# Kernel tuning notes

Measured on AMD Instinct MI355X. Metric: run time of the kernel, lower is better.

The kernel has to match this reference:

```python
import jax, jax.numpy as jnp
import numpy as np
import math

B, T, DIM = 2, 2048, 4096
N_HEADS, N_KV_HEADS = 32, 8
HEAD_DIM = DIM // N_HEADS          # 128
N_REP = N_HEADS // N_KV_HEADS      # 4
ROPE_THETA = 500000.0
NEG_INF = -1e9


def setup_inputs() -> dict:
    key = jax.random.key(0)
    ks = jax.random.split(key, 5)
    x = jax.random.normal(ks[0], (B, T, DIM), dtype=jnp.float32)
    # rotary angles: theta_j = pos * base^(-2j/d), shape [T, HEAD_DIM//2]
    inv_freq = 1.0 / (ROPE_THETA ** (jnp.arange(0, HEAD_DIM, 2, dtype=jnp.float32) / HEAD_DIM))
    freqs = jnp.arange(T, dtype=jnp.float32)[:, None] * inv_freq[None, :]
    # causal additive mask [T, T]
    mask = jnp.where(jnp.tril(jnp.ones((T, T), dtype=bool)), 0.0, NEG_INF).astype(jnp.float32)
    s = 0.02
    wq = jax.random.normal(ks[1], (DIM, N_HEADS * HEAD_DIM), dtype=jnp.float32) * s
    wk = jax.random.normal(ks[2], (DIM, N_KV_HEADS * HEAD_DIM), dtype=jnp.float32) * s
    wv = jax.random.normal(ks[3], (DIM, N_KV_HEADS * HEAD_DIM), dtype=jnp.float32) * s
    wo = jax.random.normal(ks[4], (N_HEADS * HEAD_DIM, DIM), dtype=jnp.float32) * s
    return {"x": x, "freqs": freqs, "mask": mask, "wq": wq, "wk": wk, "wv": wv, "wo": wo, "start_pos": 0}


def _apply_rope(x, cos, sin):
    # x: [B, T, H, D]; cos/sin: [T, D//2]; adjacent pairs rotated (view-as-complex)
    xr = x[..., 0::2]
    xi = x[..., 1::2]
    c = cos[None, :, None, :]
    s = sin[None, :, None, :]
    out_r = xr * c - xi * s
    out_i = xr * s + xi * c
    return jnp.stack([out_r, out_i], axis=-1).reshape(x.shape)


def reference(x, freqs, mask, wq, wk, wv, wo, start_pos):
    Bx, Tx, C = x.shape
    xq = (x @ wq).reshape(Bx, Tx, N_HEADS, HEAD_DIM)
    xk = (x @ wk).reshape(Bx, Tx, N_KV_HEADS, HEAD_DIM)
    xv = (x @ wv).reshape(Bx, Tx, N_KV_HEADS, HEAD_DIM)
    cos, sin = jnp.cos(freqs), jnp.sin(freqs)
    xq = _apply_rope(xq, cos, sin)
    xk = _apply_rope(xk, cos, sin)
    # repeat_kv for GQA: [B, T, Hkv, D] -> [B, T, Hkv*n_rep, D]
    xk = jnp.repeat(xk, N_REP, axis=2)
    xv = jnp.repeat(xv, N_REP, axis=2)
    q = xq.transpose(0, 2, 1, 3)  # [B, H, T, D]
    k = xk.transpose(0, 2, 1, 3)
    v = xv.transpose(0, 2, 1, 3)
    scores = jnp.einsum("bhtd,bhsd->bhts", q, k) / math.sqrt(HEAD_DIM)
    scores = scores + mask[None, None, :, :]
    probs = jax.nn.softmax(scores.astype(jnp.float32), axis=-1).astype(q.dtype)
    out = jnp.einsum("bhts,bhsd->bhtd", probs, v)
    out = out.transpose(0, 2, 1, 3).reshape(Bx, Tx, -1)
    return out @ wo
```

## Files before the change

### kernel.cpp

```cpp
#include <hip/hip_runtime.h>
#include <cstdint>
#include <cstddef>

typedef float  f32x4  __attribute__((ext_vector_type(4)));
typedef short  bf16x8 __attribute__((ext_vector_type(8)));
typedef unsigned short u16;
typedef u16    u16x8  __attribute__((ext_vector_type(8)));
typedef unsigned int u32;

#define T_SEQ 2048
#define N_HEADS 32
#define N_KVH 8
#define HD 128
#define QSCALE 0.12751743648963412f

__device__ __forceinline__ u16 f2bf(float f){
  union { float f; unsigned u; } v; v.f = f;
  unsigned u = v.u;
  u += 0x7fffu + ((u >> 16) & 1u);
  return (u16)(u >> 16);
}

__device__ __forceinline__ u32 cvt_pk_bf16(float a, float b){
  u32 r;
  asm volatile("v_cvt_pk_bf16_f32 %0, %1, %2" : "=v"(r) : "v"(a), "v"(b));
  return r;
}

__device__ __forceinline__ void gll16(const void* g, void* l){
  __builtin_amdgcn_global_load_lds((const __attribute__((address_space(1))) void*)g,
                                   (__attribute__((address_space(3))) void*)l, 16, 0, 0);
}

__global__ void mk_tables(const float* __restrict__ f, float* __restrict__ c, float* __restrict__ s,
                          float* __restrict__ ct, float* __restrict__ st){
  int i = blockIdx.x*256 + threadIdx.x;
  float v = f[i];
  float cv = cosf(v), sv = sinf(v);
  c[i] = cv;
  s[i] = sv;
  int t = i >> 6, d = i & 63;
  ct[d*T_SEQ + t] = cv;
  st[d*T_SEQ + t] = sv;
}

__global__ void cvt_bf16(const float* __restrict__ in, u16* __restrict__ out){
  size_t i = (size_t)blockIdx.x*256 + threadIdx.x;
  const float4* p = (const float4*)(in + i*8);
  float4 a = p[0], b = p[1];
  u16x8 o;
  o[0]=f2bf(a.x); o[1]=f2bf(a.y); o[2]=f2bf(a.z); o[3]=f2bf(a.w);
  o[4]=f2bf(b.x); o[5]=f2bf(b.y); o[6]=f2bf(b.z); o[7]=f2bf(b.w);
  *(u16x8*)(out + i*8) = o;
}

__global__ void wtrans(const float* __restrict__ W, u16* __restrict__ Wt, int K, int N){
  __shared__ float t[32][33];
  int tx = threadIdx.x, ty = threadIdx.y;
  int nb = blockIdx.x*32, kb = blockIdx.y*32;
#pragma unroll
  for (int j=0;j<4;j++) t[ty+8*j][tx] = W[(size_t)(kb+ty+8*j)*N + nb + tx];
  __syncthreads();
#pragma unroll
  for (int j=0;j<4;j++) Wt[(size_t)(nb+ty+8*j)*K + kb + tx] = f2bf(t[tx][ty+8*j]);
}

template<int BN>
__global__ __launch_bounds__(512, 2) void gemm256(
    const u16* __restrict__ A, const u16* __restrict__ Bt,
    float* __restrict__ C, int N, int K)
{
  constexpr int NGB = BN/64;
  constexpr int NF  = BN/64;
  __shared__ u16 Ab[2][16384];
  __shared__ u16 Bb[2][BN*64];
  const int tid = threadIdx.x;
  const int w = tid >> 6, lane = tid & 63;
  const int lo = lane & 15, hi = lane >> 4;

  const int nbx = N / BN;
  const int cpx = (int)gridDim.x >> 3;
  const int swzb = ((int)blockIdx.x & 7)*cpx + ((int)blockIdx.x >> 3);
  const int bx = swzb % nbx, by = swzb / nbx;
  const int m0 = by << 8, n0 = bx * BN;
  const int wm = w >> 2, wn = w & 3;

  const int rA = tid >> 3;
  const int chg = (tid & 7) ^ (rA & 7);
  const size_t srcoff = (size_t)rA * K + chg*8;
  const u16* Ag = A  + (size_t)m0*K + srcoff;
  const u16* Bg = Bt + (size_t)n0*K + srcoff;
  const int dstc = (w*64)*8;

  f32x4 acc[8][NF];
#pragma unroll
  for (int i=0;i<8;i++)
#pragma unroll
    for (int j=0;j<NF;j++) acc[i][j] = (f32x4){0.f,0.f,0.f,0.f};

  const int NT = K >> 6;
#pragma unroll
  for (int j=0;j<4;j++)   gll16(Ag + (size_t)j*64*K, &Ab[0][j*4096 + dstc]);
#pragma unroll
  for (int j=0;j<NGB;j++) gll16(Bg + (size_t)j*64*K, &Bb[0][j*4096 + dstc]);

  const int sw = lo & 7;
#pragma unroll 1
  for (int t=0; t<NT; ++t){
    const int cur = t & 1;
    if (t > 0){
      asm volatile("s_waitcnt lgkmcnt(0)" ::: "memory");
      __builtin_amdgcn_s_barrier();
    }
    if (t + 1 < NT){
      const int kt = (t+1) << 6;
      const int nxt = cur ^ 1;
#pragma unroll
      for (int j=0;j<4;j++)   gll16(Ag + (size_t)j*64*K + kt, &Ab[nxt][j*4096 + dstc]);
#pragma unroll
      for (int j=0;j<NGB;j++) gll16(Bg + (size_t)j*64*K + kt, &Bb[nxt][j*4096 + dstc]);
      if constexpr (BN == 256){
        asm volatile("s_waitcnt vmcnt(8)" ::: "memory");
      } else {
        asm volatile("s_waitcnt vmcnt(6)" ::: "memory");
      }
    } else {
      asm volatile("s_waitcnt vmcnt(0)" ::: "memory");
    }
    __builtin_amdgcn_s_barrier();
    __builtin_amdgcn_sched_barrier(0);

    const u16* Ac = &Ab[cur][0] + (wm*128)*64;
    const u16* Bc = &Bb[cur][0] + (wn*(BN/4))*64;
    bf16x8 a[4], b[NF];
#pragma unroll
    for (int ks=0; ks<2; ks++){
      const int ch = ((ks*4 + hi) ^ sw) << 3;
#pragma unroll
      for (int g=0; g<NF; g++) b[g] = *(const bf16x8*)(Bc + (g*16 + lo)*64 + ch);
#pragma unroll
      for (int mh=0; mh<2; mh++){
#pragma unroll
        for (int f=0; f<4; f++) a[f] = *(const bf16x8*)(Ac + (mh*64 + f*16 + lo)*64 + ch);
        __builtin_amdgcn_s_setprio(1);
#pragma unroll
        for (int f=0; f<4; f++)
#pragma unroll
          for (int g=0; g<NF; g++)
            acc[mh*4+f][g] = __builtin_amdgcn_mfma_f32_16x16x32_bf16(a[f], b[g], acc[mh*4+f][g], 0, 0, 0);
        __builtin_amdgcn_s_setprio(0);
      }
    }
  }

#pragma unroll
  for (int mh=0; mh<2; mh++)
#pragma unroll
    for (int f=0; f<4; f++)
#pragma unroll
      for (int g=0; g<NF; g++)
#pragma unroll
        for (int r=0; r<4; r++)
          C[(size_t)(m0 + wm*128 + mh*64 + f*16 + hi*4 + r)*N + n0 + wn*(BN/4) + g*16 + lo] = acc[mh*4+f][g][r];
}

#define DSA8(MH, RG) { _Pragma("unroll") for (int f=0; f<4; f++) a[f] = *(const bf16x8*)(AL + (RG) + La[MH][f]); }
#define DSB8(RG)     { _Pragma("unroll") for (int g=0; g<4; g++) b[g] = *(const bf16x8*)(BL + (RG) + Lb[g]); }
#define STGA8(RG, KO) { gll16(Ag + offs0 + (KO), AL + (RG) + wofs); gll16(Ag + offs1 + (KO), AL + (RG) + 4096 + wofs); }
#define STGB8(RG, KO) { gll16(Bg + offs0 + (KO), BL + (RG) + wofs); gll16(Bg + offs1 + (KO), BL + (RG) + 4096 + wofs); }
#define MFMA16(MH) { _Pragma("unroll") for (int f=0; f<4; f++) _Pragma("unroll") for (int g=0; g<4; g++) \
    acc[(MH)*4+f][g] = __builtin_amdgcn_mfma_f32_16x16x32_bf16(a[f], b[g], acc[(MH)*4+f][g], 0, 0, 0); }
#define PH_SYNC() { __builtin_amdgcn_sched_barrier(0); __builtin_amdgcn_s_barrier(); \
    asm volatile("s_waitcnt lgkmcnt(0)" ::: "memory"); __builtin_amdgcn_sched_barrier(0); }
#define PH_END() { __builtin_amdgcn_s_setprio(0); __builtin_amdgcn_s_barrier(); }

__global__ __launch_bounds__(512, 2) void gemm8p(
    const u16* __restrict__ A, const u16* __restrict__ Bt,
    float* __restrict__ C, int N, int K)
{
  __shared__ u16 AL[32768];
  __shared__ u16 BL[32768];
  const int tid = threadIdx.x;
  const int w = tid >> 6, lane = tid & 63;
  const int lo = lane & 15, hi = lane >> 4;

  const int nbx = N >> 8;
  const int cpx = (int)gridDim.x >> 3;
  const int swzb = ((int)blockIdx.x & 7)*cpx + ((int)blockIdx.x >> 3);
  const int bx = swzb % nbx, by = swzb / nbx;
  const int m0 = by << 8, n0 = bx << 8;
  const int wm = w >> 2, wn = w & 3;

  int La[2][4], Lb[4];
#pragma unroll
  for (int mh=0; mh<2; mh++)
#pragma unroll
    for (int f=0; f<4; f++){
      int row = wm*128 + mh*64 + f*16 + lo;
      int p = row >> 1;
      La[mh][f] = (p*8 + (((row&1)*4 + hi) ^ (p&7)))*8;
    }
#pragma unroll
  for (int g=0; g<4; g++){
    int row = wn*64 + g*16 + lo;
    int p = row >> 1;
    Lb[g] = (p*8 + (((row&1)*4 + hi) ^ (p&7)))*8;
  }

  int offs0, offs1;
  {
    int n = tid;
    int p = n>>3, e = (n&7) ^ (p&7);
    offs0 = (p*2 + (e>>2))*K + (e&3)*8;
    n = 512 + tid;
    p = n>>3; e = (n&7) ^ (p&7);
    offs1 = (p*2 + (e>>2))*K + (e&3)*8;
  }
  const u16* Ag = A  + (size_t)m0*K;
  const u16* Bg = Bt + (size_t)n0*K;
  const int wofs = w*512;

  f32x4 acc[8][4];
#pragma unroll
  for (int i=0;i<8;i++)
#pragma unroll
    for (int j=0;j<4;j++) acc[i][j] = (f32x4){0.f,0.f,0.f,0.f};

  const int NT = K >> 6;
  bf16x8 a[4], b[4];

  STGA8(0, 0)       STGB8(0, 0)
  STGA8(8192, 32)   STGB8(8192, 32)
  STGA8(16384, 64)  STGB8(16384, 64)
  asm volatile("s_waitcnt vmcnt(8)" ::: "memory");
  __builtin_amdgcn_s_barrier();

#pragma unroll 1
  for (int u = 0; u < NT-2; u += 2){
    const int ku = u*64;
    DSA8(0, 0) DSB8(0)
    STGA8(24576, ku+96)
    PH_SYNC() __builtin_amdgcn_s_setprio(1); MFMA16(0) PH_END()
    DSA8(1, 0)
    STGB8(24576, ku+96)
    asm volatile("s_waitcnt vmcnt(8)" ::: "memory");
    PH_SYNC() __builtin_amdgcn_s_setprio(1); MFMA16(1) PH_END()
    DSA8(0, 8192) DSB8(8192)
    STGA8(0, ku+128)
    PH_SYNC() __builtin_amdgcn_s_setprio(1); MFMA16(0) PH_END()
    DSA8(1, 8192)
    STGB8(0, ku+128)
    asm volatile("s_waitcnt vmcnt(8)" ::: "memory");
    PH_SYNC() __builtin_amdgcn_s_setprio(1); MFMA16(1) PH_END()
    DSA8(0, 16384) DSB8(16384)
    STGA8(8192, ku+160)
    PH_SYNC() __builtin_amdgcn_s_setprio(1); MFMA16(0) PH_END()
    DSA8(1, 16384)
    STGB8(8192, ku+160)
    asm volatile("s_waitcnt vmcnt(8)" ::: "memory");
    PH_SYNC() __builtin_amdgcn_s_setprio(1); MFMA16(1) PH_END()
    DSA8(0, 24576) DSB8(24576)
    STGA8(16384, ku+192)
    PH_SYNC() __builtin_amdgcn_s_setprio(1); MFMA16(0) PH_END()
    DSA8(1, 24576)
    STGB8(16384, ku+192)
    asm volatile("s_waitcnt vmcnt(8)" ::: "memory");
    PH_SYNC() __builtin_amdgcn_s_setprio(1); MFMA16(1) PH_END()
  }

  {
    const int ku = (NT-2)*64;
    DSA8(0, 0) DSB8(0)
    STGA8(24576, ku+96)
    PH_SYNC() __builtin_amdgcn_s_setprio(1); MFMA16(0) PH_END()
    DSA8(1, 0)
    STGB8(24576, ku+96)
    asm volatile("s_waitcnt vmcnt(8)" ::: "memory");
    PH_SYNC() __builtin_amdgcn_s_setprio(1); MFMA16(1) PH_END()
    DSA8(0, 8192) DSB8(8192)
    PH_SYNC() __builtin_amdgcn_s_setprio(1); MFMA16(0) PH_END()
    DSA8(1, 8192)
    asm volatile("s_waitcnt vmcnt(4)" ::: "memory");
    PH_SYNC() __builtin_amdgcn_s_setprio(1); MFMA16(1) PH_END()
    DSA8(0, 16384) DSB8(16384)
    PH_SYNC() __builtin_amdgcn_s_setprio(1); MFMA16(0) PH_END()
    DSA8(1, 16384)
    asm volatile("s_waitcnt vmcnt(0)" ::: "memory");
    PH_SYNC() __builtin_amdgcn_s_setprio(1); MFMA16(1) PH_END()
    DSA8(0, 24576) DSB8(24576)
    PH_SYNC() __builtin_amdgcn_s_setprio(1); MFMA16(0) PH_END()
    DSA8(1, 24576)
    PH_SYNC() __builtin_amdgcn_s_setprio(1); MFMA16(1) PH_END()
  }

#pragma unroll
  for (int mh=0; mh<2; mh++)
#pragma unroll
    for (int f=0; f<4; f++)
#pragma unroll
      for (int g=0; g<4; g++)
#pragma unroll
        for (int r=0; r<4; r++)
          C[(size_t)(m0 + wm*128 + mh*64 + f*16 + hi*4 + r)*N + n0 + wn*64 + g*16 + lo] = acc[mh*4+f][g][r];
}

__global__ void rope_k(const float* __restrict__ kvf, const float* __restrict__ c,
                       const float* __restrict__ s, u16* __restrict__ kb){
  const int row = blockIdx.x;
  const int b = row >> 11, t = row & (T_SEQ-1);
  const float* ib = kvf + (size_t)row*2048;
#pragma unroll
  for (int k=0;k<2;k++){
    int p = threadIdx.x + k*256;
    int kvh = p >> 6, i = p & 63;
    float cv = c[t*64+i], sv = s[t*64+i];
    float2 v = *(const float2*)(ib + 2*p);
    float vr = v.x*cv - v.y*sv;
    float vi = v.x*sv + v.y*cv;
    u16* o = kb + ((size_t)(b*N_KVH+kvh)*T_SEQ + t)*HD + 2*i;
    ushort2 ov; ov.x = f2bf(vr); ov.y = f2bf(vi);
    *(ushort2*)o = ov;
  }
}

__global__ void vtrans(const float* __restrict__ kvf, u16* __restrict__ vt){
  __shared__ float tl[32][33];
  int tx = threadIdx.x, ty = threadIdx.y;
  int t0 = blockIdx.x*32, d0 = blockIdx.y*32, bh = blockIdx.z;
  int b = bh >> 3, kvh = bh & 7;
#pragma unroll
  for (int j=0;j<4;j++)
    tl[ty+8*j][tx] = kvf[(size_t)(b*T_SEQ + t0+ty+8*j)*2048 + 1024 + kvh*HD + d0 + tx];
  __syncthreads();
#pragma unroll
  for (int j=0;j<4;j++)
    vt[((size_t)bh*HD + d0+ty+8*j)*T_SEQ + t0 + tx] = f2bf(tl[tx][ty+8*j]);
}

#define KVB 64
__global__ __launch_bounds__(512) void attn_kernel(
    const float* __restrict__ qf, const float* __restrict__ costT, const float* __restrict__ sintT,
    const u16* __restrict__ kb, const u16* __restrict__ vt, u16* __restrict__ attn)
{
  __shared__ u16 KV[2][2][8192];

  const int tid = threadIdx.x;
  const int lane = tid & 63, wid = tid >> 6;
  const int lo = lane & 15, hi = lane >> 4;
  const bool lowhi = (hi < 2);
  const int bp0 = lo + 32*(hi & 1);
  const int bp1 = bp0 + 16;
  const int h = blockIdx.y, b = blockIdx.z;
  const int kvh = h >> 2;
  const int qt = b ? (int)blockIdx.x : 7 - (int)blockIdx.x;
  const int q0 = qt*256 + wid*32;
  const int ntiles = (qt+1)*4;

  int koff[2], voff[2];
#pragma unroll
  for (int p=0;p<2;p++){
    int s = p*512 + tid;
    int kr = s >> 4, kch = (s & 15) ^ (kr & 7);
    koff[p] = kr*HD + kch*8;
    int vd = s >> 3, vch = (s & 7) ^ (vd & 7);
    voff[p] = vd*T_SEQ + vch*8;
  }
  const u16* Kg = kb + (size_t)(b*N_KVH + kvh)*T_SEQ*HD;
  const u16* Vg = vt + (size_t)(b*N_KVH + kvh)*HD*T_SEQ;

  bf16x8 qfr[2][4];
#pragma unroll
  for (int mb=0;mb<2;mb++){
    const int t = q0 + mb*16 + lo;
    const float* qrow = qf + (size_t)(b*T_SEQ + t)*4096 + h*HD;
#pragma unroll
    for (int kc=0;kc<4;kc++){
      f32x4 v0 = *(const f32x4*)(qrow + kc*32 + hi*8);
      f32x4 v1 = *(const f32x4*)(qrow + kc*32 + hi*8 + 4);
      union { u32 w[4]; bf16x8 v; } pk;
#pragma unroll
      for (int j=0;j<4;j++){
        int i = kc*16 + hi*4 + j;
        float cv = costT[i*T_SEQ + t], sv = sintT[i*T_SEQ + t];
        float xr = (j<2) ? v0[2*j]   : v1[2*(j-2)];
        float xi = (j<2) ? v0[2*j+1] : v1[2*(j-2)+1];
        float vr = (xr*cv - xi*sv)*QSCALE;
        float vi = (xr*sv + xi*cv)*QSCALE;
        pk.w[j] = ((u32)f2bf(vi) << 16) | (u32)f2bf(vr);
      }
      qfr[mb][kc] = pk.v;
    }
  }

  f32x4 acc[2][8];
#pragma unroll
  for (int mb=0;mb<2;mb++)
#pragma unroll
    for (int nd=0;nd<8;nd++) acc[mb][nd] = (f32x4){0.f,0.f,0.f,0.f};
  float m_[2] = {-3.0e38f, -3.0e38f};
  float l_[2] = {0.f, 0.f};

#pragma unroll
  for (int p=0;p<2;p++){
    gll16(Kg + koff[p], (u16*)&KV[0][0][0] + (p*512 + wid*64)*8);
    gll16(Vg + voff[p], (u16*)&KV[0][1][0] + (p*512 + wid*64)*8);
  }

#pragma unroll 1
  for (int st=0; st<ntiles; ++st){
    const int cur = st & 1;
    const int sb = st*KVB;
    if (st > 0){
      asm volatile("s_waitcnt lgkmcnt(0)" ::: "memory");
      __builtin_amdgcn_s_barrier();
    }
    if (st + 1 < ntiles){
      const int nxt = cur ^ 1;
      const int nb2 = (st+1)*KVB;
#pragma unroll
      for (int p=0;p<2;p++){
        gll16(Kg + nb2*HD + koff[p], (u16*)&KV[nxt][0][0] + (p*512 + wid*64)*8);
        gll16(Vg + nb2    + voff[p], (u16*)&KV[nxt][1][0] + (p*512 + wid*64)*8);
      }
      asm volatile("s_waitcnt vmcnt(4)" ::: "memory");
    } else {
      asm volatile("s_waitcnt vmcnt(0)" ::: "memory");
    }
    __builtin_amdgcn_s_barrier();

    const bool live = (sb <= q0 + 31);
    if (live){
      f32x4 sc[2][4];
#pragma unroll
      for (int mb=0;mb<2;mb++)
#pragma unroll
        for (int ns=0;ns<4;ns++) sc[mb][ns] = (f32x4){0.f,0.f,0.f,0.f};
      __builtin_amdgcn_s_setprio(1);
#pragma unroll
      for (int ns=0;ns<4;ns++){
        const int row = ns*16 + lo;
        const u16* klp = (const u16*)&KV[cur][0][0] + row*HD;
        const int sw = row & 7;
        bf16x8 kf[4];
#pragma unroll
        for (int kc=0;kc<4;kc++) kf[kc] = *(const bf16x8*)(klp + (((kc*4+hi)^sw)<<3));
#pragma unroll
        for (int kc=0;kc<4;kc++){
          sc[0][ns] = __builtin_amdgcn_mfma_f32_16x16x32_bf16(kf[kc], qfr[0][kc], sc[0][ns], 0, 0, 0);
          sc[1][ns] = __builtin_amdgcn_mfma_f32_16x16x32_bf16(kf[kc], qfr[1][kc], sc[1][ns], 0, 0, 0);
        }
      }
      __builtin_amdgcn_s_setprio(0);

      if (sb + 63 > q0){
#pragma unroll
        for (int mb=0;mb<2;mb++){
          const int qg = q0 + mb*16 + lo;
#pragma unroll
          for (int ns=0;ns<4;ns++)
#pragma unroll
            for (int r=0;r<4;r++){
              int sg = sb + ns*16 + hi*4 + r;
              if (sg > qg) sc[mb][ns][r] = -3.0e38f;
            }
        }
      }

      bf16x8 pa[2][2];
#pragma unroll
      for (int mb=0;mb<2;mb++){
        float mx = fmaxf(fmaxf(fmaxf(sc[mb][0][0],sc[mb][0][1]),fmaxf(sc[mb][0][2],sc[mb][0][3])),
                   fmaxf(fmaxf(fmaxf(sc[mb][1][0],sc[mb][1][1]),fmaxf(sc[mb][1][2],sc[mb][1][3])),
                         fmaxf(fmaxf(sc[mb][2][0],sc[mb][2][1]),
                               fmaxf(fmaxf(sc[mb][2][2],sc[mb][2][3]),
                                     fmaxf(fmaxf(sc[mb][3][0],sc[mb][3][1]),fmaxf(sc[mb][3][2],sc[mb][3][3]))))));
        mx = fmaxf(mx, __shfl_xor(mx, 16));
        mx = fmaxf(mx, __shfl_xor(mx, 32));
        if (__any(mx > m_[mb] + 8.f)){
          float mn = fmaxf(m_[mb], mx);
          float scal = exp2f(m_[mb] - mn);
          m_[mb] = mn;
          l_[mb] *= scal;
          float srow[4];
#pragma unroll
          for (int r=0;r<4;r++) srow[r] = __shfl(scal, hi*4+r);
#pragma unroll
          for (int nd=0;nd<8;nd++)
#pragma unroll
            for (int r=0;r<4;r++) acc[mb][nd][r] *= srow[r];
        }
        float rs = 0.f;
#pragma unroll
        for (int ns=0;ns<4;ns++)
#pragma unroll
          for (int r=0;r<4;r++){
            sc[mb][ns][r] = exp2f(sc[mb][ns][r] - m_[mb]);
            rs += sc[mb][ns][r];
          }
        rs += __shfl_xor(rs, 16);
        rs += __shfl_xor(rs, 32);
        l_[mb] += rs;

#pragma unroll
        for (int k2=0;k2<2;k2++){
          u32 P0 = cvt_pk_bf16(sc[mb][2*k2][0],   sc[mb][2*k2][1]);
          u32 P1 = cvt_pk_bf16(sc[mb][2*k2][2],   sc[mb][2*k2][3]);
          u32 Q0 = cvt_pk_bf16(sc[mb][2*k2+1][0], sc[mb][2*k2+1][1]);
          u32 Q1 = cvt_pk_bf16(sc[mb][2*k2+1][2], sc[mb][2*k2+1][3]);
          u32 pA0 = (u32)__shfl((int)P0, bp0);
          u32 pA1 = (u32)__shfl((int)P1, bp0);
          u32 pA2 = (u32)__shfl((int)P0, bp1);
          u32 pA3 = (u32)__shfl((int)P1, bp1);
          u32 qA0 = (u32)__shfl((int)Q0, bp0);
          u32 qA1 = (u32)__shfl((int)Q1, bp0);
          u32 qA2 = (u32)__shfl((int)Q0, bp1);
          u32 qA3 = (u32)__shfl((int)Q1, bp1);
          union { u32 w[4]; bf16x8 v; } pk;
          pk.w[0] = lowhi ? pA0 : qA0;
          pk.w[1] = lowhi ? pA1 : qA1;
          pk.w[2] = lowhi ? pA2 : qA2;
          pk.w[3] = lowhi ? pA3 : qA3;
          pa[mb][k2] = pk.v;
        }
      }

      __builtin_amdgcn_s_setprio(1);
#pragma unroll
      for (int nd=0;nd<8;nd++){
        const int d = nd*16 + lo;
        const u16* vlp = (const u16*)&KV[cur][1][0] + d*64;
        const int sw = d & 7;
        bf16x8 vf[2];
#pragma unroll
        for (int k2=0;k2<2;k2++) vf[k2] = *(const bf16x8*)(vlp + (((k2*4+hi)^sw)<<3));
#pragma unroll
        for (int k2=0;k2<2;k2++){
          acc[0][nd] = __builtin_amdgcn_mfma_f32_16x16x32_bf16(pa[0][k2], vf[k2], acc[0][nd], 0, 0, 0);
          acc[1][nd] = __builtin_amdgcn_mfma_f32_16x16x32_bf16(pa[1][k2], vf[k2], acc[1][nd], 0, 0, 0);
        }
      }
      __builtin_amdgcn_s_setprio(0);
    }
  }

#pragma unroll
  for (int mb=0;mb<2;mb++){
    float inv = 1.f / l_[mb];
    float invr[4];
#pragma unroll
    for (int r=0;r<4;r++) invr[r] = __shfl(inv, hi*4+r);
    u16* ob = attn + (size_t)(b*T_SEQ + q0 + mb*16 + hi*4)*4096 + h*HD;
#pragma unroll
    for (int nd=0;nd<8;nd++)
#pragma unroll
      for (int r=0;r<4;r++)
        ob[(size_t)r*4096 + nd*16 + lo] = f2bf(acc[mb][nd][r]*invr[r]);
  }
}

extern "C" void kernel_launch(void* const* d_in, const int* in_sizes, int n_in,
                              void* d_out, int out_size, void* d_ws, size_t ws_size,
                              hipStream_t stream)
{
  (void)in_sizes; (void)n_in; (void)out_size; (void)ws_size;
  const float* x     = (const float*)d_in[0];
  const float* freqs = (const float*)d_in[1];
  const float* wq    = (const float*)d_in[3];
  const float* wk    = (const float*)d_in[4];
  const float* wv    = (const float*)d_in[5];
  const float* wo    = (const float*)d_in[6];

  char* ws = (char*)d_ws;
  float* cost  = (float*)(ws + 0);
  float* sint  = (float*)(ws + 524288);
  u16* xb   = (u16*)(ws + 1048576);
  u16* wqt  = (u16*)(ws + 34603008);
  u16* wkt  = (u16*)(ws + 68157440);
  u16* wvt  = (u16*)(ws + 76546048);
  float* kvf = (float*)(ws + 84934656);
  u16* kbuf = (u16*)(ws + 118489088);
  u16* vbuf = (u16*)(ws + 126877696);
  u16* attnb = xb;
  u16* wot   = wqt;
  float* costT = (float*)(ws + 68157440);
  float* sintT = (float*)(ws + 68681728);

  float* qf = (float*)d_out;

  dim3 tb(32, 8);

  cvt_bf16<<<8192, 256, 0, stream>>>(x, xb);
  wtrans<<<dim3(128,128), tb, 0, stream>>>(wq, wqt, 4096, 4096);
  wtrans<<<dim3(32,128),  tb, 0, stream>>>(wk, wkt, 4096, 1024);
  wtrans<<<dim3(32,128),  tb, 0, stream>>>(wv, wvt, 4096, 1024);

  gemm8p<<<dim3(256), 512, 0, stream>>>(xb, wqt, qf, 4096, 4096);

  gemm256<128><<<dim3(256), 512, 0, stream>>>(xb, wkt, kvf, 2048, 4096);

  mk_tables<<<512, 256, 0, stream>>>(freqs, cost, sint, costT, sintT);

  rope_k<<<4096, 256, 0, stream>>>(kvf, cost, sint, kbuf);
  vtrans<<<dim3(64,4,16), tb, 0, stream>>>(kvf, vbuf);

  attn_kernel<<<dim3(8,32,2), 512, 0, stream>>>(qf, costT, sintT, kbuf, vbuf, attnb);

  wtrans<<<dim3(128,128), tb, 0, stream>>>(wo, wot, 4096, 4096);
  gemm8p<<<dim3(256), 512, 0, stream>>>(attnb, wot, (float*)d_out, 4096, 4096);
}
```

Before: 556.2 us.

## Double-buffer GEMM register fragments to overlap LDS reads with MFMA

Splits the A and B register fragments of the 8-phase bf16 GEMM into two ping-pong sets. Each phase now issues the LDS reads for the next phase's fragments inside the same barrier-delimited region as the current MFMA block, instead of before it. The first fragments are preloaded before the loop and the tail is reshaped to drain the pipeline. This aims to hide LDS read latency behind matrix-core work, at the cost of extra VGPRs for the second fragment set and a more delicate ordering of waits against the global-to-LDS loads.

```diff
diff --git a/kernel.cpp b/kernel.cpp
--- a/kernel.cpp
+++ b/kernel.cpp
@@ -164,15 +164,15 @@
           C[(size_t)(m0 + wm*128 + mh*64 + f*16 + hi*4 + r)*N + n0 + wn*(BN/4) + g*16 + lo] = acc[mh*4+f][g][r];
 }
 
-#define DSA8(MH, RG) { _Pragma("unroll") for (int f=0; f<4; f++) a[f] = *(const bf16x8*)(AL + (RG) + La[MH][f]); }
-#define DSB8(RG)     { _Pragma("unroll") for (int g=0; g<4; g++) b[g] = *(const bf16x8*)(BL + (RG) + Lb[g]); }
+#define RDA(BK, RG, MH) { _Pragma("unroll") for (int f=0; f<4; f++) BK[f] = *(const bf16x8*)(AL + (RG) + La[MH][f]); }
+#define RDB(BK, RG)     { _Pragma("unroll") for (int g=0; g<4; g++) BK[g] = *(const bf16x8*)(BL + (RG) + Lb[g]); }
 #define STGA8(RG, KO) { gll16(Ag + offs0 + (KO), AL + (RG) + wofs); gll16(Ag + offs1 + (KO), AL + (RG) + 4096 + wofs); }
 #define STGB8(RG, KO) { gll16(Bg + offs0 + (KO), BL + (RG) + wofs); gll16(Bg + offs1 + (KO), BL + (RG) + 4096 + wofs); }
-#define MFMA16(MH) { _Pragma("unroll") for (int f=0; f<4; f++) _Pragma("unroll") for (int g=0; g<4; g++) \
-    acc[(MH)*4+f][g] = __builtin_amdgcn_mfma_f32_16x16x32_bf16(a[f], b[g], acc[(MH)*4+f][g], 0, 0, 0); }
-#define PH_SYNC() { __builtin_amdgcn_sched_barrier(0); __builtin_amdgcn_s_barrier(); \
-    asm volatile("s_waitcnt lgkmcnt(0)" ::: "memory"); __builtin_amdgcn_sched_barrier(0); }
-#define PH_END() { __builtin_amdgcn_s_setprio(0); __builtin_amdgcn_s_barrier(); }
+#define MFMAB(AB, BB, MH) { _Pragma("unroll") for (int f=0; f<4; f++) _Pragma("unroll") for (int g=0; g<4; g++) \
+    acc[(MH)*4+f][g] = __builtin_amdgcn_mfma_f32_16x16x32_bf16(AB[f], BB[g], acc[(MH)*4+f][g], 0, 0, 0); }
+#define PH_HEAD() { __builtin_amdgcn_sched_barrier(0); __builtin_amdgcn_s_barrier(); \
+    asm volatile("s_waitcnt lgkmcnt(0)" ::: "memory"); __builtin_amdgcn_sched_barrier(0); __builtin_amdgcn_s_setprio(1); }
+#define PH_TAIL() { __builtin_amdgcn_s_setprio(0); __builtin_amdgcn_s_barrier(); }
 
 __global__ __launch_bounds__(512, 2) void gemm8p(
     const u16* __restrict__ A, const u16* __restrict__ Bt,
@@ -227,70 +227,55 @@
     for (int j=0;j<4;j++) acc[i][j] = (f32x4){0.f,0.f,0.f,0.f};
 
   const int NT = K >> 6;
-  bf16x8 a[4], b[4];
+  bf16x8 aA[4], aB[4], bA[4], bB[4];
 
   STGA8(0, 0)       STGB8(0, 0)
   STGA8(8192, 32)   STGB8(8192, 32)
   STGA8(16384, 64)  STGB8(16384, 64)
   asm volatile("s_waitcnt vmcnt(8)" ::: "memory");
   __builtin_amdgcn_s_barrier();
+  RDA(aA, 0, 0) RDB(bA, 0)
 
 #pragma unroll 1
   for (int u = 0; u < NT-2; u += 2){
     const int ku = u*64;
-    DSA8(0, 0) DSB8(0)
     STGA8(24576, ku+96)
-    PH_SYNC() __builtin_amdgcn_s_setprio(1); MFMA16(0) PH_END()
-    DSA8(1, 0)
+    PH_HEAD() RDA(aB, 0, 1) MFMAB(aA, bA, 0) PH_TAIL()
     STGB8(24576, ku+96)
     asm volatile("s_waitcnt vmcnt(8)" ::: "memory");
-    PH_SYNC() __builtin_amdgcn_s_setprio(1); MFMA16(1) PH_END()
-    DSA8(0, 8192) DSB8(8192)
+    PH_HEAD() RDA(aA, 8192, 0) RDB(bB, 8192) MFMAB(aB, bA, 1) PH_TAIL()
     STGA8(0, ku+128)
-    PH_SYNC() __builtin_amdgcn_s_setprio(1); MFMA16(0) PH_END()
-    DSA8(1, 8192)
+    PH_HEAD() RDA(aB, 8192, 1) MFMAB(aA, bB, 0) PH_TAIL()
     STGB8(0, ku+128)
     asm volatile("s_waitcnt vmcnt(8)" ::: "memory");
-    PH_SYNC() __builtin_amdgcn_s_setprio(1); MFMA16(1) PH_END()
-    DSA8(0, 16384) DSB8(16384)
+    PH_HEAD() RDA(aA, 16384, 0) RDB(bA, 16384) MFMAB(aB, bB, 1) PH_TAIL()
     STGA8(8192, ku+160)
-    PH_SYNC() __builtin_amdgcn_s_setprio(1); MFMA16(0) PH_END()
-    DSA8(1, 16384)
+    PH_HEAD() RDA(aB, 16384, 1) MFMAB(aA, bA, 0) PH_TAIL()
     STGB8(8192, ku+160)
     asm volatile("s_waitcnt vmcnt(8)" ::: "memory");
-    PH_SYNC() __builtin_amdgcn_s_setprio(1); MFMA16(1) PH_END()
-    DSA8(0, 24576) DSB8(24576)
+    PH_HEAD() RDA(aA, 24576, 0) RDB(bB, 24576) MFMAB(aB, bA, 1) PH_TAIL()
     STGA8(16384, ku+192)
-    PH_SYNC() __builtin_amdgcn_s_setprio(1); MFMA16(0) PH_END()
-    DSA8(1, 24576)
+    PH_HEAD() RDA(aB, 24576, 1) MFMAB(aA, bB, 0) PH_TAIL()
     STGB8(16384, ku+192)
     asm volatile("s_waitcnt vmcnt(8)" ::: "memory");
-    PH_SYNC() __builtin_amdgcn_s_setprio(1); MFMA16(1) PH_END()
+    PH_HEAD() RDA(aA, 0, 0) RDB(bA, 0) MFMAB(aB, bB, 1) PH_TAIL()
   }
 
   {
     const int ku = (NT-2)*64;
-    DSA8(0, 0) DSB8(0)
     STGA8(24576, ku+96)
-    PH_SYNC() __builtin_amdgcn_s_setprio(1); MFMA16(0) PH_END()
-    DSA8(1, 0)
+    PH_HEAD() RDA(aB, 0, 1) MFMAB(aA, bA, 0) PH_TAIL()
     STGB8(24576, ku+96)
     asm volatile("s_waitcnt vmcnt(8)" ::: "memory");
-    PH_SYNC() __builtin_amdgcn_s_setprio(1); MFMA16(1) PH_END()
-    DSA8(0, 8192) DSB8(8192)
-    PH_SYNC() __builtin_amdgcn_s_setprio(1); MFMA16(0) PH_END()
-    DSA8(1, 8192)
+    PH_HEAD() RDA(aA, 8192, 0) RDB(bB, 8192) MFMAB(aB, bA, 1) PH_TAIL()
+    PH_HEAD() RDA(aB, 8192, 1) MFMAB(aA, bB, 0) PH_TAIL()
     asm volatile("s_waitcnt vmcnt(4)" ::: "memory");
-    PH_SYNC() __builtin_amdgcn_s_setprio(1); MFMA16(1) PH_END()
-    DSA8(0, 16384) DSB8(16384)
-    PH_SYNC() __builtin_amdgcn_s_setprio(1); MFMA16(0) PH_END()
-    DSA8(1, 16384)
+    PH_HEAD() RDA(aA, 16384, 0) RDB(bA, 16384) MFMAB(aB, bB, 1) PH_TAIL()
+    PH_HEAD() RDA(aB, 16384, 1) MFMAB(aA, bA, 0) PH_TAIL()
     asm volatile("s_waitcnt vmcnt(0)" ::: "memory");
-    PH_SYNC() __builtin_amdgcn_s_setprio(1); MFMA16(1) PH_END()
-    DSA8(0, 24576) DSB8(24576)
-    PH_SYNC() __builtin_amdgcn_s_setprio(1); MFMA16(0) PH_END()
-    DSA8(1, 24576)
-    PH_SYNC() __builtin_amdgcn_s_setprio(1); MFMA16(1) PH_END()
+    PH_HEAD() RDA(aA, 24576, 0) RDB(bB, 24576) MFMAB(aB, bA, 1) PH_TAIL()
+    PH_HEAD() RDA(aB, 24576, 1) MFMAB(aA, bB, 0) PH_TAIL()
+    PH_HEAD() MFMAB(aB, bB, 1) PH_TAIL()
   }
 
 #pragma unroll
```

New measurement: 557.3 us. Within noise of the previous version (+0.2%).
